# Performance work log

Hardware: AMD Instinct MI355X
Metric: run time of the kernel (lower is better)

Reference implementation:

```python
import jax, jax.numpy as jnp
import numpy as np

B, T, F, H = 8, 1024, 512, 8
DK = F // H
P = 2 * T - 1  # relative position length


def setup_inputs() -> dict:
    key = jax.random.key(0)
    ks = jax.random.split(key, 16)
    s = 0.02
    inp = {
        "query": jax.random.normal(ks[0], (B, T, F), jnp.float32),
        "key": jax.random.normal(ks[1], (B, T, F), jnp.float32),
        "value": jax.random.normal(ks[2], (B, T, F), jnp.float32),
        "mask": jax.random.randint(ks[3], (B, T, T), 0, 2) > 0,
        "pos_emb": jax.random.normal(ks[4], (1, P, F), jnp.float32),
        "Wq": jax.random.normal(ks[5], (F, F), jnp.float32) * s,
        "bq": jnp.zeros((F,), jnp.float32),
        "Wk": jax.random.normal(ks[6], (F, F), jnp.float32) * s,
        "bk": jnp.zeros((F,), jnp.float32),
        "Wv": jax.random.normal(ks[7], (F, F), jnp.float32) * s,
        "bv": jnp.zeros((F,), jnp.float32),
        "Wpos": jax.random.normal(ks[8], (F, F), jnp.float32) * s,
        "Wo": jax.random.normal(ks[9], (F, F), jnp.float32) * s,
        "bo": jnp.zeros((F,), jnp.float32),
        "pos_bias_u": jax.random.normal(ks[10], (H, DK), jnp.float32) * s,
        "pos_bias_v": jax.random.normal(ks[11], (H, DK), jnp.float32) * s,
    }
    return inp


def _rel_shift(x):
    # x: (b, h, q, p) with p = 2q-1 ; Transformer-XL pad/reshape/slice trick
    b, h, q, p = x.shape
    x = jnp.pad(x, ((0, 0), (0, 0), (0, 0), (1, 0)))
    x = x.reshape(b, h, p + 1, q)[:, :, 1:, :].reshape(b, h, q, p)
    return x


def reference(query, key, value, mask, pos_emb, Wq, bq, Wk, bk, Wv, bv,
              Wpos, Wo, bo, pos_bias_u, pos_bias_v):
    b = query.shape[0]
    # projections (torch Linear: y = x @ W.T + b), split into heads -> (b,h,t,d)
    q = (query @ Wq.T + bq).reshape(b, -1, H, DK).transpose(0, 2, 1, 3)
    k = (key @ Wk.T + bk).reshape(b, -1, H, DK).transpose(0, 2, 1, 3)
    v = (value @ Wv.T + bv).reshape(b, -1, H, DK).transpose(0, 2, 1, 3)
    # positional projection: (1,P,F) -> (h,P,d)
    p = (pos_emb @ Wpos.T).reshape(-1, H, DK).transpose(1, 0, 2)

    q_u = q + pos_bias_u[None, :, None, :]
    q_v = q + pos_bias_v[None, :, None, :]

    matrix_ac = jnp.einsum("bhqd,bhkd->bhqk", q_u, k)
    matrix_bd = jnp.einsum("bhqd,hpd->bhqp", q_v, p)
    matrix_bd = _rel_shift(matrix_bd)[:, :, :, : matrix_ac.shape[-1]]

    scores = (matrix_ac + matrix_bd) / jnp.sqrt(jnp.float32(DK))
    m = mask[:, None, :, :]
    scores = jnp.where(m, -10000.0, scores)
    attn = jax.nn.softmax(scores, axis=-1)
    attn = jnp.where(m, 0.0, attn)

    x = jnp.einsum("bhqk,bhkd->bhqd", attn, v)
    x = x.transpose(0, 2, 1, 3).reshape(b, -1, H * DK)
    return x @ Wo.T + bo
```

## Files before the change

### kernel.cpp

```cpp
#include <hip/hip_runtime.h>

#define Bn 8
#define Tn 1024
#define Fn 512
#define Hn 8
#define DKn 64
#define Pn 2047

namespace {

typedef _Float16 h8 __attribute__((ext_vector_type(8)));
typedef float f4 __attribute__((ext_vector_type(4)));

__device__ __forceinline__ unsigned short f2h(float f) {
  _Float16 h = (_Float16)f;
  return __builtin_bit_cast(unsigned short, h);
}
__device__ __forceinline__ float h2f(unsigned short u) {
  return (float)__builtin_bit_cast(_Float16, u);
}

__device__ __forceinline__ f4 mfma16(h8 a, h8 b, f4 c) {
  return __builtin_amdgcn_mfma_f32_16x16x32_f16(a, b, c, 0, 0, 0);
}

__device__ __forceinline__ h8 frag_ld(const unsigned char* p, int row, int kk, int grp) {
  int off = row * 128 + kk * 64 + grp * 16;
  off ^= (row & 7) << 4;
  return *(const h8*)(p + off);
}

__device__ __forceinline__ int tile_off(int row, int d) {
  return row * 128 + (((d >> 3) << 4) ^ ((row & 7) << 4)) + (d & 7) * 2;
}

__device__ __forceinline__ void tload(const unsigned char* img, int t, uint4& a, uint4& b) {
  a = *(const uint4*)(img + t * 16);
  b = *(const uint4*)(img + 4096 + t * 16);
}
__device__ __forceinline__ void tstore(unsigned char* s, int t, const uint4& a, const uint4& b) {
  *(uint4*)(s + t * 16) = a;
  *(uint4*)(s + 4096 + t * 16) = b;
}

__global__ void detect_kernel(const unsigned int* m, int* flag) {
  if (threadIdx.x == 0) {
    int bm = 0;
    for (int i = 0; i < 256; ++i)
      if (m[i] > 1u) bm = 1;
    *flag = bm;
  }
}

__global__ __launch_bounds__(256) void maskbits_kernel(
    const void* __restrict__ maskp, const int* __restrict__ flagp,
    unsigned long long* __restrict__ Mb) {
  const int wid = (blockIdx.x * 256 + threadIdx.x) >> 6;
  const int l = threadIdx.x & 63;
  const int byte_mode = *flagp;
  const size_t base = (size_t)wid * Tn;
  for (int kt = 0; kt < 16; ++kt) {
    bool mv;
    if (byte_mode)
      mv = ((const unsigned char*)maskp)[base + kt * 64 + l] != 0;
    else
      mv = ((const int*)maskp)[base + kt * 64 + l] != 0;
    unsigned long long bits = __ballot(mv);
    if (l == 0) Mb[(size_t)wid * 16 + kt] = bits;
  }
}

__global__ __launch_bounds__(256) void qkvp_kernel(
    const float* __restrict__ Aq, const float* __restrict__ Ak,
    const float* __restrict__ Av, const float* __restrict__ Ap,
    const float* __restrict__ Wq, const float* __restrict__ Wk,
    const float* __restrict__ Wv, const float* __restrict__ Wp,
    const float* __restrict__ bq, const float* __restrict__ bk,
    const float* __restrict__ bv,
    const float* __restrict__ pbu, const float* __restrict__ pbv,
    unsigned short* __restrict__ Qu, unsigned short* __restrict__ Qv,
    unsigned char* __restrict__ Kws, unsigned char* __restrict__ Vws,
    unsigned char* __restrict__ Pws) {
  const int mode = blockIdx.z;
  if (mode == 3 && blockIdx.x >= 32) return;
  const float* A = mode == 0 ? Aq : mode == 1 ? Ak : mode == 2 ? Av : Ap;
  const float* W = mode == 0 ? Wq : mode == 1 ? Wk : mode == 2 ? Wv : Wp;
  const float* bias = mode == 0 ? bq : mode == 1 ? bk : bv;
  const int M = mode == 3 ? Pn : Bn * Tn;

  __shared__ __align__(16) unsigned char sA[64 * 128];
  __shared__ __align__(16) unsigned char sB[64 * 128];

  const int t = threadIdx.x;
  const int w = t >> 6, l = t & 63;
  const int grp = l >> 4, lc = l & 15;
  const int m0 = blockIdx.x * 64, n0 = blockIdx.y * 64;
  const int srow = t >> 2, sseg = t & 3;

  f4 acc[4];
#pragma unroll
  for (int c = 0; c < 4; ++c) acc[c] = {0.f, 0.f, 0.f, 0.f};

  for (int kt = 0; kt < 8; ++kt) {
    {
      int gm = m0 + srow;
      int sw = (srow & 7) << 4;
      bool valid = (gm < M);
      const float* ar = A + (size_t)gm * Fn + kt * 64 + sseg * 16;
#pragma unroll
      for (int i = 0; i < 4; ++i) {
        float4 fv = valid ? *(const float4*)(ar + 4 * i) : make_float4(0.f, 0.f, 0.f, 0.f);
        uint2 pk;
        pk.x = (unsigned)f2h(fv.x) | ((unsigned)f2h(fv.y) << 16);
        pk.y = (unsigned)f2h(fv.z) | ((unsigned)f2h(fv.w) << 16);
        int off = srow * 128 + sseg * 32 + i * 8;
        *(uint2*)(sA + (off ^ sw)) = pk;
      }
      const float* br = W + (size_t)(n0 + srow) * Fn + kt * 64 + sseg * 16;
#pragma unroll
      for (int i = 0; i < 4; ++i) {
        float4 fv = *(const float4*)(br + 4 * i);
        uint2 pk;
        pk.x = (unsigned)f2h(fv.x) | ((unsigned)f2h(fv.y) << 16);
        pk.y = (unsigned)f2h(fv.z) | ((unsigned)f2h(fv.w) << 16);
        int off = srow * 128 + sseg * 32 + i * 8;
        *(uint2*)(sB + (off ^ sw)) = pk;
      }
    }
    __syncthreads();
    const int arow = 16 * w + lc;
    h8 a0 = frag_ld(sA, arow, 0, grp);
    h8 a1 = frag_ld(sA, arow, 1, grp);
#pragma unroll
    for (int c = 0; c < 4; ++c) {
      int brow = 16 * c + lc;
      acc[c] = mfma16(a0, frag_ld(sB, brow, 0, grp), acc[c]);
      acc[c] = mfma16(a1, frag_ld(sB, brow, 1, grp), acc[c]);
    }
    __syncthreads();
  }

#pragma unroll
  for (int c = 0; c < 4; ++c) {
#pragma unroll
    for (int r = 0; r < 4; ++r) {
      int m = m0 + 16 * w + grp * 4 + r;
      int n = n0 + 16 * c + lc;
      float vv = acc[c][r];
      if (mode == 0) {
        vv += bias[n];
        int b = m >> 10, tt = m & 1023, h = n >> 6, d = n & 63;
        size_t qi = ((size_t)(b * Hn + h) * Tn + tt) * DKn + d;
        Qu[qi] = f2h(vv + pbu[n]);
        Qv[qi] = f2h(vv + pbv[n]);
      } else if (mode == 1) {
        vv += bias[n];
        int b = m >> 10, tt = m & 1023, h = n >> 6, d = n & 63;
        size_t off = (((size_t)(b * Hn + h) * 16 + (tt >> 6)) << 13) + tile_off(tt & 63, d);
        *(unsigned short*)(Kws + off) = f2h(vv);
      } else if (mode == 2) {
        vv += bias[n];
        int b = m >> 10, tt = m & 1023, h = n >> 6, d = n & 63;
        size_t off = (((size_t)(b * Hn + h) * 16 + (tt >> 6)) << 13) + tile_off(d, tt & 63);
        *(unsigned short*)(Vws + off) = f2h(vv);
      } else {
        int h = n >> 6, d = n & 63;
        size_t off = (((size_t)h * 32 + (m >> 6)) << 13) + tile_off(m & 63, d);
        *(unsigned short*)(Pws + off) = f2h(m < M ? vv : 0.f);
      }
    }
  }
}

__global__ __launch_bounds__(256) void oproj_kernel(
    const unsigned short* __restrict__ Ah, const float* __restrict__ W,
    const float* __restrict__ bias, float* __restrict__ ofp) {
  __shared__ __align__(16) unsigned char sA[64 * 128];
  __shared__ __align__(16) unsigned char sB[64 * 128];

  const int t = threadIdx.x;
  const int w = t >> 6, l = t & 63;
  const int grp = l >> 4, lc = l & 15;
  const int m0 = blockIdx.x * 64, n0 = blockIdx.y * 64;
  const int srow = t >> 2, sseg = t & 3;

  f4 acc[4];
#pragma unroll
  for (int c = 0; c < 4; ++c) acc[c] = {0.f, 0.f, 0.f, 0.f};

  for (int kt = 0; kt < 8; ++kt) {
    {
      int gm = m0 + srow;
      int sw = (srow & 7) << 4;
      const unsigned short* ar = Ah + (size_t)gm * Fn + kt * 64 + sseg * 16;
#pragma unroll
      for (int hh = 0; hh < 2; ++hh) {
        uint4 qd = *(const uint4*)(ar + hh * 8);
        int off = srow * 128 + sseg * 32 + hh * 16;
        *(uint2*)(sA + ((off) ^ sw)) = make_uint2(qd.x, qd.y);
        *(uint2*)(sA + ((off + 8) ^ sw)) = make_uint2(qd.z, qd.w);
      }
      const float* br = W + (size_t)(n0 + srow) * Fn + kt * 64 + sseg * 16;
#pragma unroll
      for (int i = 0; i < 4; ++i) {
        float4 fv = *(const float4*)(br + 4 * i);
        uint2 pk;
        pk.x = (unsigned)f2h(fv.x) | ((unsigned)f2h(fv.y) << 16);
        pk.y = (unsigned)f2h(fv.z) | ((unsigned)f2h(fv.w) << 16);
        int off = srow * 128 + sseg * 32 + i * 8;
        *(uint2*)(sB + (off ^ sw)) = pk;
      }
    }
    __syncthreads();
    const int arow = 16 * w + lc;
    h8 a0 = frag_ld(sA, arow, 0, grp);
    h8 a1 = frag_ld(sA, arow, 1, grp);
#pragma unroll
    for (int c = 0; c < 4; ++c) {
      int brow = 16 * c + lc;
      acc[c] = mfma16(a0, frag_ld(sB, brow, 0, grp), acc[c]);
      acc[c] = mfma16(a1, frag_ld(sB, brow, 1, grp), acc[c]);
    }
    __syncthreads();
  }

#pragma unroll
  for (int c = 0; c < 4; ++c) {
#pragma unroll
    for (int r = 0; r < 4; ++r) {
      int m = m0 + 16 * w + grp * 4 + r;
      int n = 16 * c + lc + n0;
      ofp[(size_t)m * Fn + n] = acc[c][r] + bias[n];
    }
  }
}

__global__ __launch_bounds__(256, 3) void attn_kernel(
    const unsigned short* __restrict__ Qu, const unsigned short* __restrict__ Qv,
    const unsigned char* __restrict__ Kws, const unsigned char* __restrict__ Vws,
    const unsigned char* __restrict__ Pws, const unsigned long long* __restrict__ Mb,
    unsigned short* __restrict__ xb) {
  __shared__ __align__(16) unsigned char smem[52480];

  const int t = threadIdx.x;
  const int w = t >> 6, l = t & 63;
  const int grp = l >> 4, lc = l & 15;
  const int q0 = blockIdx.x * 64;
  const int bh = blockIdx.y;
  const int b = bh >> 3, h = bh & 7;

  unsigned char* sK = smem;
  unsigned char* sV = smem + 8192;
  unsigned char* sP = smem + 16384;
  unsigned char* bdw = smem + 32768 + w * 2880;
  unsigned char* ppw = smem + 44288 + w * 2048;

  const unsigned char* Kg = Kws + ((size_t)bh << 17);
  const unsigned char* Vg = Vws + ((size_t)bh << 17);
  const unsigned char* Pg = Pws + ((size_t)h << 18);
  const int s0 = 15 - (q0 >> 6);

  h8 au[2], av[2];
  {
    const size_t qbase = ((size_t)bh * Tn + q0 + 16 * w + lc) * DKn;
#pragma unroll
    for (int kk = 0; kk < 2; ++kk) {
      au[kk] = *(const h8*)(Qu + qbase + kk * 32 + grp * 8);
      av[kk] = *(const h8*)(Qv + qbase + kk * 32 + grp * 8);
    }
  }

  {
    uint4 ka, kb, va, vb, pa, pb, pc, pd;
    tload(Kg, t, ka, kb);
    tload(Vg, t, va, vb);
    tload(Pg + ((size_t)s0 << 13), t, pa, pb);
    tload(Pg + ((size_t)(s0 + 1) << 13), t, pc, pd);
    tstore(sK, t, ka, kb);
    tstore(sV, t, va, vb);
    tstore(sP + ((s0 & 1) << 13), t, pa, pb);
    tstore(sP + (((s0 + 1) & 1) << 13), t, pc, pd);
  }
  __syncthreads();

  float m_run[4], l_run[4];
  f4 oacc[4];
#pragma unroll
  for (int r = 0; r < 4; ++r) { m_run[r] = -1e30f; l_run[r] = 0.f; }
#pragma unroll
  for (int c = 0; c < 4; ++c) oacc[c] = {0.f, 0.f, 0.f, 0.f};

  const size_t mrowbase = ((size_t)(b << 10) + q0 + 16 * w) * 16;

  for (int kt = 0; kt < 16; ++kt) {
    const int k0 = kt * 64;
    const bool more = kt < 15;

    uint4 ka, kb, va, vb, pa, pb;
    if (more) {
      tload(Kg + ((size_t)(kt + 1) << 13), t, ka, kb);
      tload(Vg + ((size_t)(kt + 1) << 13), t, va, vb);
      tload(Pg + ((size_t)(s0 + kt + 2) << 13), t, pa, pb);
    }

    f4 ac[4];
#pragma unroll
    for (int c = 0; c < 4; ++c) {
      int brow = 16 * c + lc;
      ac[c] = {0.f, 0.f, 0.f, 0.f};
      ac[c] = mfma16(au[0], frag_ld(sK, brow, 0, grp), ac[c]);
      ac[c] = mfma16(au[1], frag_ld(sK, brow, 1, grp), ac[c]);
    }

    const int pbase = k0 - q0 + 960;
    const int wbase = 48 - 16 * w;
#pragma unroll
    for (int c2 = 0; c2 < 5; ++c2) {
      int prow0 = pbase + wbase + 16 * c2;
      const unsigned char* slot = sP + ((((unsigned)prow0 >> 6) & 1) << 13);
      int rloc = prow0 & 63;
      f4 z = {0.f, 0.f, 0.f, 0.f};
      z = mfma16(av[0], frag_ld(slot, rloc + lc, 0, grp), z);
      z = mfma16(av[1], frag_ld(slot, rloc + lc, 1, grp), z);
      unsigned lo = (unsigned)f2h(z[0]) | ((unsigned)f2h(z[1]) << 16);
      unsigned hi = (unsigned)f2h(z[2]) | ((unsigned)f2h(z[3]) << 16);
      unsigned char* dst = bdw + (size_t)(((16 * c2 + lc) * 18 + grp * 4) * 2);
      *(unsigned*)dst = lo;
      *(unsigned*)(dst + 4) = hi;
    }

#pragma unroll
    for (int r = 0; r < 4; ++r) {
      const int rr = grp * 4 + r;
      const unsigned long long m64 = Mb[mrowbase + (size_t)rr * 16 + kt];
      float sc[4];
#pragma unroll
      for (int c = 0; c < 4; ++c) {
        const int col = 16 * c + lc;
        float bdf = h2f(*(const unsigned short*)(bdw + (size_t)(((col - rr + 15) * 18 + rr) * 2)));
        float vv = (ac[c][r] + bdf) * 0.18033688f;
        sc[c] = ((m64 >> col) & 1ull) ? -14427.0f : vv;
      }
      float mx = fmaxf(fmaxf(sc[0], sc[1]), fmaxf(sc[2], sc[3]));
#pragma unroll
      for (int d2 = 1; d2 < 16; d2 <<= 1) mx = fmaxf(mx, __shfl_xor(mx, d2, 64));
      float mnew = fmaxf(m_run[r], mx);
      float scl = exp2f(m_run[r] - mnew);
      float ps = 0.f;
      unsigned short ph[4];
#pragma unroll
      for (int c = 0; c < 4; ++c) {
        float p = exp2f(sc[c] - mnew);
        ps += p;
        ph[c] = f2h(p);
      }
#pragma unroll
      for (int d2 = 1; d2 < 16; d2 <<= 1) ps += __shfl_xor(ps, d2, 64);
      l_run[r] = l_run[r] * scl + ps;
      m_run[r] = mnew;
#pragma unroll
      for (int c = 0; c < 4; ++c) oacc[c][r] *= scl;
      const int sw = (rr & 7) << 4;
#pragma unroll
      for (int c = 0; c < 4; ++c) {
        int off = (rr * 128 + (16 * c + lc) * 2) ^ sw;
        *(unsigned short*)(ppw + off) = ph[c];
      }
    }

    {
      h8 pa0 = frag_ld(ppw, lc, 0, grp);
      h8 pa1 = frag_ld(ppw, lc, 1, grp);
#pragma unroll
      for (int c = 0; c < 4; ++c) {
        int brow = 16 * c + lc;
        oacc[c] = mfma16(pa0, frag_ld(sV, brow, 0, grp), oacc[c]);
        oacc[c] = mfma16(pa1, frag_ld(sV, brow, 1, grp), oacc[c]);
      }
    }

    if (more) {
      __syncthreads();
      tstore(sK, t, ka, kb);
      tstore(sV, t, va, vb);
      tstore(sP + (((s0 + kt) & 1) << 13), t, pa, pb);
      __syncthreads();
    }
  }

#pragma unroll
  for (int c = 0; c < 4; ++c) {
#pragma unroll
    for (int r = 0; r < 4; ++r) {
      int rowq = 16 * w + grp * 4 + r;
      float vv = oacc[c][r] / l_run[r];
      size_t idx = ((size_t)b * Tn + q0 + rowq) * Fn + h * DKn + 16 * c + lc;
      xb[idx] = f2h(vv);
    }
  }
}

}

extern "C" void kernel_launch(void* const* d_in, const int* in_sizes, int n_in,
                              void* d_out, int out_size, void* d_ws, size_t ws_size,
                              hipStream_t stream) {
  const float* query = (const float*)d_in[0];
  const float* key = (const float*)d_in[1];
  const float* value = (const float*)d_in[2];
  const void* maskp = d_in[3];
  const float* pos = (const float*)d_in[4];
  const float* Wq = (const float*)d_in[5];
  const float* bq = (const float*)d_in[6];
  const float* Wk = (const float*)d_in[7];
  const float* bk = (const float*)d_in[8];
  const float* Wv = (const float*)d_in[9];
  const float* bv = (const float*)d_in[10];
  const float* Wpos = (const float*)d_in[11];
  const float* Wo = (const float*)d_in[12];
  const float* bo = (const float*)d_in[13];
  const float* pu = (const float*)d_in[14];
  const float* pv = (const float*)d_in[15];
  float* out = (float*)d_out;

  unsigned char* ws = (unsigned char*)d_ws;
  int* flag = (int*)ws;
  size_t o = 256;
  unsigned long long* Mb = (unsigned long long*)(ws + o); o += (size_t)Bn * Tn * 16 * 8;
  unsigned short* Qu = (unsigned short*)(ws + o); o += (size_t)Bn * Hn * Tn * DKn * 2;
  unsigned short* Qv = (unsigned short*)(ws + o); o += (size_t)Bn * Hn * Tn * DKn * 2;
  unsigned char* Kws = ws + o; o += (size_t)Bn * Hn * 16 * 8192;
  unsigned char* Vws = ws + o; o += (size_t)Bn * Hn * 16 * 8192;
  unsigned char* Pws = ws + o; o += (size_t)Hn * 32 * 8192;
  unsigned short* xb = (unsigned short*)(ws + o);

  detect_kernel<<<dim3(1), dim3(64), 0, stream>>>((const unsigned int*)maskp, flag);
  maskbits_kernel<<<dim3(2048), dim3(256), 0, stream>>>(maskp, flag, Mb);
  qkvp_kernel<<<dim3(128, 8, 4), dim3(256), 0, stream>>>(
      query, key, value, pos, Wq, Wk, Wv, Wpos, bq, bk, bv, pu, pv,
      Qu, Qv, Kws, Vws, Pws);
  attn_kernel<<<dim3(16, 64), dim3(256), 0, stream>>>(Qu, Qv, Kws, Vws, Pws, Mb, xb);
  oproj_kernel<<<dim3(128, 8), dim3(256), 0, stream>>>(xb, Wo, bo, out);
}
```

Baseline: 216.2 us.

## Pre-convert weights to fp16 once and swizzle attention block order

Adds a small kernel that converts all five weight matrices to fp16 in workspace once per call, so the projection GEMMs load half-width weights instead of re-reading and re-converting fp32 weights in every tile. The attention launch becomes a 1D grid whose block index is remapped so that consecutive blocks spread across batch-heads and query tiles. The remap is meant to improve cache sharing of K, V and positional tiles across XCDs. The cost is one extra launch plus a 2.5MB workspace write and read.

```diff
diff --git a/kernel.cpp b/kernel.cpp
--- a/kernel.cpp
+++ b/kernel.cpp
@@ -70,11 +70,28 @@
   }
 }
 
+__global__ __launch_bounds__(256) void wcvt_kernel(
+    const float* __restrict__ W0, const float* __restrict__ W1,
+    const float* __restrict__ W2, const float* __restrict__ W3,
+    const float* __restrict__ W4, unsigned short* __restrict__ Whs) {
+  const float* src = blockIdx.y == 0 ? W0 : blockIdx.y == 1 ? W1
+                    : blockIdx.y == 2 ? W2 : blockIdx.y == 3 ? W3 : W4;
+  unsigned short* dst = Whs + (size_t)blockIdx.y * 262144;
+  int i = (blockIdx.x * 256 + threadIdx.x) * 8;
+  float4 a = *(const float4*)(src + i);
+  float4 b = *(const float4*)(src + i + 4);
+  uint4 o;
+  o.x = (unsigned)f2h(a.x) | ((unsigned)f2h(a.y) << 16);
+  o.y = (unsigned)f2h(a.z) | ((unsigned)f2h(a.w) << 16);
+  o.z = (unsigned)f2h(b.x) | ((unsigned)f2h(b.y) << 16);
+  o.w = (unsigned)f2h(b.z) | ((unsigned)f2h(b.w) << 16);
+  *(uint4*)(dst + i) = o;
+}
+
 __global__ __launch_bounds__(256) void qkvp_kernel(
     const float* __restrict__ Aq, const float* __restrict__ Ak,
     const float* __restrict__ Av, const float* __restrict__ Ap,
-    const float* __restrict__ Wq, const float* __restrict__ Wk,
-    const float* __restrict__ Wv, const float* __restrict__ Wp,
+    const unsigned short* __restrict__ Whs,
     const float* __restrict__ bq, const float* __restrict__ bk,
     const float* __restrict__ bv,
     const float* __restrict__ pbu, const float* __restrict__ pbv,
@@ -84,7 +101,7 @@
   const int mode = blockIdx.z;
   if (mode == 3 && blockIdx.x >= 32) return;
   const float* A = mode == 0 ? Aq : mode == 1 ? Ak : mode == 2 ? Av : Ap;
-  const float* W = mode == 0 ? Wq : mode == 1 ? Wk : mode == 2 ? Wv : Wp;
+  const unsigned short* Wh = Whs + (size_t)mode * 262144;
   const float* bias = mode == 0 ? bq : mode == 1 ? bk : bv;
   const int M = mode == 3 ? Pn : Bn * Tn;
 
@@ -116,15 +133,13 @@
         int off = srow * 128 + sseg * 32 + i * 8;
         *(uint2*)(sA + (off ^ sw)) = pk;
       }
-      const float* br = W + (size_t)(n0 + srow) * Fn + kt * 64 + sseg * 16;
-#pragma unroll
-      for (int i = 0; i < 4; ++i) {
-        float4 fv = *(const float4*)(br + 4 * i);
-        uint2 pk;
-        pk.x = (unsigned)f2h(fv.x) | ((unsigned)f2h(fv.y) << 16);
-        pk.y = (unsigned)f2h(fv.z) | ((unsigned)f2h(fv.w) << 16);
-        int off = srow * 128 + sseg * 32 + i * 8;
-        *(uint2*)(sB + (off ^ sw)) = pk;
+      const unsigned short* br = Wh + (size_t)(n0 + srow) * Fn + kt * 64 + sseg * 16;
+#pragma unroll
+      for (int hh = 0; hh < 2; ++hh) {
+        uint4 qd = *(const uint4*)(br + hh * 8);
+        int off = srow * 128 + sseg * 32 + hh * 16;
+        *(uint2*)(sB + ((off) ^ sw)) = make_uint2(qd.x, qd.y);
+        *(uint2*)(sB + ((off + 8) ^ sw)) = make_uint2(qd.z, qd.w);
       }
     }
     __syncthreads();
@@ -173,7 +188,7 @@
 }
 
 __global__ __launch_bounds__(256) void oproj_kernel(
-    const unsigned short* __restrict__ Ah, const float* __restrict__ W,
+    const unsigned short* __restrict__ Ah, const unsigned short* __restrict__ Wh,
     const float* __restrict__ bias, float* __restrict__ ofp) {
   __shared__ __align__(16) unsigned char sA[64 * 128];
   __shared__ __align__(16) unsigned char sB[64 * 128];
@@ -190,9 +205,8 @@
 
   for (int kt = 0; kt < 8; ++kt) {
     {
-      int gm = m0 + srow;
       int sw = (srow & 7) << 4;
-      const unsigned short* ar = Ah + (size_t)gm * Fn + kt * 64 + sseg * 16;
+      const unsigned short* ar = Ah + (size_t)(m0 + srow) * Fn + kt * 64 + sseg * 16;
 #pragma unroll
       for (int hh = 0; hh < 2; ++hh) {
         uint4 qd = *(const uint4*)(ar + hh * 8);
@@ -200,15 +214,13 @@
         *(uint2*)(sA + ((off) ^ sw)) = make_uint2(qd.x, qd.y);
         *(uint2*)(sA + ((off + 8) ^ sw)) = make_uint2(qd.z, qd.w);
       }
-      const float* br = W + (size_t)(n0 + srow) * Fn + kt * 64 + sseg * 16;
-#pragma unroll
-      for (int i = 0; i < 4; ++i) {
-        float4 fv = *(const float4*)(br + 4 * i);
-        uint2 pk;
-        pk.x = (unsigned)f2h(fv.x) | ((unsigned)f2h(fv.y) << 16);
-        pk.y = (unsigned)f2h(fv.z) | ((unsigned)f2h(fv.w) << 16);
-        int off = srow * 128 + sseg * 32 + i * 8;
-        *(uint2*)(sB + (off ^ sw)) = pk;
+      const unsigned short* br = Wh + (size_t)(n0 + srow) * Fn + kt * 64 + sseg * 16;
+#pragma unroll
+      for (int hh = 0; hh < 2; ++hh) {
+        uint4 qd = *(const uint4*)(br + hh * 8);
+        int off = srow * 128 + sseg * 32 + hh * 16;
+        *(uint2*)(sB + ((off) ^ sw)) = make_uint2(qd.x, qd.y);
+        *(uint2*)(sB + ((off + 8) ^ sw)) = make_uint2(qd.z, qd.w);
       }
     }
     __syncthreads();
@@ -245,8 +257,10 @@
   const int t = threadIdx.x;
   const int w = t >> 6, l = t & 63;
   const int grp = l >> 4, lc = l & 15;
-  const int q0 = blockIdx.x * 64;
-  const int bh = blockIdx.y;
+  const int lin = blockIdx.x;
+  const int swz = (lin & 7) * 128 + (lin >> 3);
+  const int q0 = (swz & 15) * 64;
+  const int bh = swz >> 4;
   const int b = bh >> 3, h = bh & 7;
 
   unsigned char* sK = smem;
@@ -426,6 +440,7 @@
   unsigned char* ws = (unsigned char*)d_ws;
   int* flag = (int*)ws;
   size_t o = 256;
+  unsigned short* Whs = (unsigned short*)(ws + o); o += (size_t)5 * 262144 * 2;
   unsigned long long* Mb = (unsigned long long*)(ws + o); o += (size_t)Bn * Tn * 16 * 8;
   unsigned short* Qu = (unsigned short*)(ws + o); o += (size_t)Bn * Hn * Tn * DKn * 2;
   unsigned short* Qv = (unsigned short*)(ws + o); o += (size_t)Bn * Hn * Tn * DKn * 2;
@@ -436,9 +451,10 @@
 
   detect_kernel<<<dim3(1), dim3(64), 0, stream>>>((const unsigned int*)maskp, flag);
   maskbits_kernel<<<dim3(2048), dim3(256), 0, stream>>>(maskp, flag, Mb);
+  wcvt_kernel<<<dim3(128, 5), dim3(256), 0, stream>>>(Wq, Wk, Wv, Wpos, Wo, Whs);
   qkvp_kernel<<<dim3(128, 8, 4), dim3(256), 0, stream>>>(
-      query, key, value, pos, Wq, Wk, Wv, Wpos, bq, bk, bv, pu, pv,
+      query, key, value, pos, Whs, bq, bk, bv, pu, pv,
       Qu, Qv, Kws, Vws, Pws);
-  attn_kernel<<<dim3(16, 64), dim3(256), 0, stream>>>(Qu, Qv, Kws, Vws, Pws, Mb, xb);
-  oproj_kernel<<<dim3(128, 8), dim3(256), 0, stream>>>(xb, Wo, bo, out);
-}
+  attn_kernel<<<dim3(1024), dim3(256), 0, stream>>>(Qu, Qv, Kws, Vws, Pws, Mb, xb);
+  oproj_kernel<<<dim3(128, 8), dim3(256), 0, stream>>>(xb, Whs + 4 * 262144, bo, out);
+}
```

New measurement: 195.3 us (median of 3 runs). -9.7%, faster.
